# Performance work log

Hardware: AMD Instinct MI355X
Metric: run time of the kernel (lower is better)

Reference implementation:

```python
import jax, jax.numpy as jnp
import numpy as np

B, TX, TY = 32, 64, 64
E = H = 1024
VEN = VCN = 32000


def _lstm_scan(x_gates, Whh, bhh, h0, c0):
    # x_gates: [T, B, 4H] precomputed input contribution (x @ Wih.T + bih)
    def step(carry, xg_t):
        h, c = carry
        gates = xg_t + h @ Whh.T + bhh  # [B, 4H]
        i, f, g, o = jnp.split(gates, 4, axis=-1)  # torch gate order i,f,g,o
        c = jax.nn.sigmoid(f) * c + jax.nn.sigmoid(i) * jnp.tanh(g)
        h = jax.nn.sigmoid(o) * jnp.tanh(c)
        return (h, c), (h, c)
    (hT, cT), (hs, cs) = jax.lax.scan(step, (h0, c0), x_gates)
    return hs, cs, hT, cT  # hs/cs: [T, B, H]


def setup_inputs() -> dict:
    key = jax.random.key(0)
    ks = jax.random.split(key, 12)
    u = lambda k, shp, s: jax.random.uniform(k, shp, jnp.float32, -s, s)
    s = 1.0 / np.sqrt(H)
    return {
        "x": jax.random.randint(ks[0], (B, TX), 0, VEN, dtype=jnp.int32),
        "x_mask": jnp.ones((B, TX), dtype=jnp.int32),
        "y": jax.random.randint(ks[1], (B, TY), 0, VCN, dtype=jnp.int32),
        "h0": jnp.zeros((B, H), jnp.float32),
        "c0": jnp.zeros((B, H), jnp.float32),
        "emb_en": u(ks[2], (VEN, E), 0.1),
        "emb_cn": u(ks[3], (VCN, E), 0.1),
        "Wih_e": u(ks[4], (4 * H, E), s),
        "Whh_e": u(ks[5], (4 * H, H), s),
        "bih_e": jnp.zeros((4 * H,), jnp.float32),
        "bhh_e": jnp.zeros((4 * H,), jnp.float32),
        "Wih_d": u(ks[6], (4 * H, E), s),
        "Whh_d": u(ks[7], (4 * H, H), s),
        "bih_d": jnp.zeros((4 * H,), jnp.float32),
        "bhh_d": jnp.zeros((4 * H,), jnp.float32),
        "Wout": u(ks[8], (VCN, H), 0.1),
        "bout": jnp.zeros((VCN,), jnp.float32),
    }


def reference(x, x_mask, y, h0, c0, emb_en, emb_cn,
              Wih_e, Whh_e, bih_e, bhh_e,
              Wih_d, Whh_d, bih_d, bhh_d, Wout, bout):
    # --- encoder: per-timestep LSTMCell unrolled via lax.scan ---
    xe = emb_en[x]  # [B, Tx, E]
    xg = jnp.einsum('bte,ge->tbg', xe, Wih_e) + bih_e  # [Tx, B, 4H]
    hs, cs, _, _ = _lstm_scan(xg, Whh_e, bhh_e, h0, c0)  # [Tx, B, H]
    # pick hidden/cell at last valid timestep (mask.sum - 1)
    lengths = jnp.sum(x_mask, axis=1) - 1  # [B]
    bidx = jnp.arange(x.shape[0])
    h = hs[lengths, bidx]  # [B, H]
    c = cs[lengths, bidx]
    # --- decoder: single-layer LSTM ---
    ye = emb_cn[y]  # [B, Ty, E]
    yg = jnp.einsum('bte,ge->tbg', ye, Wih_d) + bih_d  # [Ty, B, 4H]
    dh, _, _, _ = _lstm_scan(yg, Whh_d, bhh_d, h, c)  # [Ty, B, H]
    hiddens = jnp.transpose(dh, (1, 0, 2))  # [B, Ty, H]
    logits = jnp.einsum('bth,vh->btv', hiddens, Wout) + bout  # [B, Ty, V]
    decoded = jax.nn.log_softmax(logits, axis=-1)
    return decoded, hiddens
```

## Files before the change

### kernel.cpp

```cpp
#include <hip/hip_runtime.h>

typedef __attribute__((ext_vector_type(8))) short bf16x8;
typedef __attribute__((ext_vector_type(4))) float fx4;
typedef __attribute__((ext_vector_type(4))) unsigned short u16x4;
typedef __attribute__((ext_vector_type(8))) unsigned short u16x8;
typedef __attribute__((ext_vector_type(4))) unsigned int u32x4;

#define DEV static __device__ __forceinline__

DEV unsigned short f2bf(float f) {
  union { float f; unsigned u; } v; v.f = f;
  unsigned u = v.u;
  u += 0x7fffu + ((u >> 16) & 1u);
  return (unsigned short)(u >> 16);
}
DEV unsigned pk(float a, float b) { return (unsigned)f2bf(a) | ((unsigned)f2bf(b) << 16); }
DEV float sigm(float x) { return 1.f / (1.f + __expf(-x)); }

DEV u32x4 load_coh16(const void* p) {
  u32x4 r;
  asm volatile("global_load_dwordx4 %0, %1, off sc0 sc1" : "=v"(r) : "v"(p));
  return r;
}

typedef __attribute__((address_space(1))) const unsigned int guint;
typedef __attribute__((address_space(3))) unsigned int luint;
DEV void gload_lds16(const void* g, void* l) {
  __builtin_amdgcn_global_load_lds((guint*)g, (luint*)l, 16, 0, 0);
}

__global__ void k_gather2(const float* __restrict__ embE, const int* __restrict__ tokE,
                          unsigned short* __restrict__ dstE,
                          const float* __restrict__ embC, const int* __restrict__ tokC,
                          unsigned short* __restrict__ dstC) {
  int bid = blockIdx.x;
  int r = bid & 2047;
  const float* emb = bid < 2048 ? embE : embC;
  const int* tok = bid < 2048 ? tokE : tokC;
  unsigned short* dst = bid < 2048 ? dstE : dstC;
  int t = r >> 5, b = r & 31;
  int token = tok[b * 64 + t];
  const fx4* srow = (const fx4*)(emb + (long)token * 1024);
  u16x4* drow = (u16x4*)(dst + (long)r * 1024);
  fx4 v = srow[threadIdx.x];
  u16x4 o = { f2bf(v[0]), f2bf(v[1]), f2bf(v[2]), f2bf(v[3]) };
  drow[threadIdx.x] = o;
}

__global__ void k_lengths(const int* __restrict__ mask, int* __restrict__ sel,
                          int* __restrict__ bar) {
  int t = threadIdx.x;
  for (int i = t; i < 4096; i += 256) bar[i] = 0;
  if (t < 32) {
    int s = 0;
    for (int k = 0; k < 64; ++k) s += mask[t * 64 + k];
    sel[t] = (s + 63) & 63;
  }
}

__global__ void k_f2bf_dual(const float* __restrict__ s0, unsigned short* __restrict__ d0,
                            const float* __restrict__ s1, unsigned short* __restrict__ d1,
                            long n4) {
  const float* s = blockIdx.x < 1024 ? s0 : s1;
  unsigned short* d = blockIdx.x < 1024 ? d0 : d1;
  long base = (long)(blockIdx.x & 1023) * 256 + threadIdx.x;
  for (long i = base; i < n4; i += 1024 * 256) {
    fx4 v = ((const fx4*)s)[i];
    u16x4 o = { f2bf(v[0]), f2bf(v[1]), f2bf(v[2]), f2bf(v[3]) };
    ((u16x4*)d)[i] = o;
  }
}

#define SCAN_NBLK 64

__global__ __launch_bounds__(512) void k_scan_all(
    const float* __restrict__ WhhE, const float* __restrict__ bhhE,
    const float* __restrict__ xg_e,
    const float* __restrict__ WhhD, const float* __restrict__ bhhD,
    const float* __restrict__ xg_d,
    const float* __restrict__ h0, const float* __restrict__ c0,
    unsigned short* __restrict__ hbuf,
    const int* __restrict__ sel,
    float* __restrict__ hid_out,
    unsigned short* __restrict__ hid_bf,
    int* __restrict__ bar,
    const float* __restrict__ wsrc,
    unsigned short* __restrict__ wdst,
    long wn4) {
  int tid = threadIdx.x;
  int bid = blockIdx.x;
  if (bid >= SCAN_NBLK) {
    long i = (long)(bid - SCAN_NBLK) * 512 + tid;
    long st = (long)(gridDim.x - SCAN_NBLK) * 512;
    for (; i < wn4; i += st) {
      fx4 v = ((const fx4*)wsrc)[i];
      u16x4 o = { f2bf(v[0]), f2bf(v[1]), f2bf(v[2]), f2bf(v[3]) };
      ((u16x4*)wdst)[i] = o;
    }
    return;
  }
  __shared__ __align__(16) unsigned short hlds[49152];
  __shared__ float gbuf[4][32][16];
  int j0 = ((bid & 7) * 8 + (bid >> 3)) * 16;
  int w = tid >> 6, lane = tid & 63;
  int mt = w & 1, nt = w >> 1;
  int fr = lane & 15, fg = lane >> 4;
  unsigned* hbU = (unsigned*)hbuf;

  auto gridbar = [&](int gen) {
    __syncthreads();
    if (w == 0) {
      if (lane == 0)
        __hip_atomic_store(&bar[bid * 32], gen, __ATOMIC_RELAXED, __HIP_MEMORY_SCOPE_AGENT);
      for (;;) {
        int v0 = __hip_atomic_load(&bar[lane * 32], __ATOMIC_RELAXED, __HIP_MEMORY_SCOPE_AGENT);
        if (__ballot(v0 >= gen) == 0xFFFFFFFFFFFFFFFFULL) break;
        __builtin_amdgcn_s_sleep(1);
      }
    }
    __syncthreads();
  };

  auto loadBreg = [&](const float* Whh, bf16x8* breg) {
    const float* wrow = Whh + ((long)(nt * 1024 + j0 + fr) << 10);
#pragma unroll
    for (int i = 0; i < 32; ++i) {
      int kc = i * 4 + fg;
      fx4 lo = *(const fx4*)(wrow + kc * 8);
      fx4 hi = *(const fx4*)(wrow + kc * 8 + 4);
      bf16x8 o = { (short)f2bf(lo[0]), (short)f2bf(lo[1]), (short)f2bf(lo[2]), (short)f2bf(lo[3]),
                   (short)f2bf(hi[0]), (short)f2bf(hi[1]), (short)f2bf(hi[2]), (short)f2bf(hi[3]) };
      breg[i] = o;
    }
  };

  bf16x8 breg[32];
  loadBreg(WhhE, breg);

  int b = tid >> 4, jj = tid & 15, j = j0 + jj;
  float bh0 = bhhE[j], bh1 = bhhE[1024 + j], bh2 = bhhE[2048 + j], bh3 = bhhE[3072 + j];
  float c_reg = c0[b * 1024 + j];
  int sel_b = sel[b];
  float hsel_reg = 0.f, csel_reg = 0.f;
  const float* xp0 = xg_e + (long)b * 4096 + j;
  float x0 = xp0[0], x1 = xp0[1024], x2 = xp0[2048], x3 = xp0[3072];

  for (int t = 0; t < 64; ++t) {
    if (t == 0) {
#pragma unroll
      for (int it = 0; it < 8; ++it) {
        int c = it * 512 + tid;
        const float* src = h0 + (long)c * 8;
        fx4 lo = *(const fx4*)src;
        fx4 hi = *(const fx4*)(src + 4);
        int row = c >> 7, kc = c & 127;
        u16x8 o = { f2bf(lo[0]), f2bf(lo[1]), f2bf(lo[2]), f2bf(lo[3]),
                    f2bf(hi[0]), f2bf(hi[1]), f2bf(hi[2]), f2bf(hi[3]) };
        *(u16x8*)&hlds[(row * 128 + (kc ^ (row & 31))) * 8] = o;
      }
    } else {
      const char* hsrc = (const char*)hbuf + (t & 1) * 65536;
      u32x4 hv[8];
#pragma unroll
      for (int it = 0; it < 8; ++it) {
        int c = it * 512 + tid;
        hv[it] = load_coh16(hsrc + (long)c * 16);
      }
      asm volatile("s_waitcnt vmcnt(0)" ::: "memory");
      __builtin_amdgcn_sched_barrier(0);
#pragma unroll
      for (int it = 0; it < 8; ++it) {
        int c = it * 512 + tid;
        int row = c >> 7, kc = c & 127;
        *(u16x8*)&hlds[(row * 128 + (kc ^ (row & 31))) * 8] = *(u16x8*)&hv[it];
      }
    }
    __syncthreads();

    int arow = mt * 16 + fr;
    fx4 acca = {0.f, 0.f, 0.f, 0.f}, accb = {0.f, 0.f, 0.f, 0.f};
#pragma unroll
    for (int i = 0; i < 32; i += 2) {
      int kcA = i * 4 + fg, kcB = (i + 1) * 4 + fg;
      bf16x8 a0 = *(const bf16x8*)&hlds[(arow * 128 + (kcA ^ (arow & 31))) * 8];
      bf16x8 a1 = *(const bf16x8*)&hlds[(arow * 128 + (kcB ^ (arow & 31))) * 8];
      acca = __builtin_amdgcn_mfma_f32_16x16x32_bf16(a0, breg[i], acca, 0, 0, 0);
      accb = __builtin_amdgcn_mfma_f32_16x16x32_bf16(a1, breg[i + 1], accb, 0, 0, 0);
    }
#pragma unroll
    for (int q = 0; q < 4; ++q)
      gbuf[nt][mt * 16 + fg * 4 + q][fr] = acca[q] + accb[q];
    __syncthreads();

    {
      float gi = gbuf[0][b][jj] + bh0 + x0;
      float gf = gbuf[1][b][jj] + bh1 + x1;
      float gg = gbuf[2][b][jj] + bh2 + x2;
      float go = gbuf[3][b][jj] + bh3 + x3;
      float c_new = sigm(gf) * c_reg + sigm(gi) * tanhf(gg);
      float h = sigm(go) * tanhf(c_new);
      c_reg = c_new;
      float hp = __shfl_xor(h, 1);
      if ((jj & 1) == 0) {
        __hip_atomic_store(&hbU[((t & 1) ^ 1) * 16384 + b * 512 + ((j0 + jj) >> 1)],
                           pk(h, hp), __ATOMIC_RELAXED, __HIP_MEMORY_SCOPE_AGENT);
      }
      if (t == sel_b) { hsel_reg = h; csel_reg = c_new; }
    }

    if (t < 63) {
      const float* xp = xg_e + (long)(t + 1) * 131072 + (long)b * 4096 + j;
      float nx0 = xp[0], nx1 = xp[1024], nx2 = xp[2048], nx3 = xp[3072];
      gridbar(t + 1);
      x0 = nx0; x1 = nx1; x2 = nx2; x3 = nx3;
    }
  }

  loadBreg(WhhD, breg);
  bh0 = bhhD[j]; bh1 = bhhD[1024 + j]; bh2 = bhhD[2048 + j]; bh3 = bhhD[3072 + j];
  c_reg = csel_reg;
  {
    float hp = __shfl_xor(hsel_reg, 1);
    if ((jj & 1) == 0)
      __hip_atomic_store(&hbU[b * 512 + ((j0 + jj) >> 1)],
                         pk(hsel_reg, hp), __ATOMIC_RELAXED, __HIP_MEMORY_SCOPE_AGENT);
  }
  {
    const float* xp = xg_d + (long)b * 4096 + j;
    x0 = xp[0]; x1 = xp[1024]; x2 = xp[2048]; x3 = xp[3072];
  }
  gridbar(64);

  for (int t2 = 0; t2 < 64; ++t2) {
    const char* hsrc = (const char*)hbuf + (t2 & 1) * 65536;
    u32x4 hv[8];
#pragma unroll
    for (int it = 0; it < 8; ++it) {
      int c = it * 512 + tid;
      hv[it] = load_coh16(hsrc + (long)c * 16);
    }
    asm volatile("s_waitcnt vmcnt(0)" ::: "memory");
    __builtin_amdgcn_sched_barrier(0);
#pragma unroll
    for (int it = 0; it < 8; ++it) {
      int c = it * 512 + tid;
      int row = c >> 7, kc = c & 127;
      *(u16x8*)&hlds[(row * 128 + (kc ^ (row & 31))) * 8] = *(u16x8*)&hv[it];
    }
    __syncthreads();

    int arow = mt * 16 + fr;
    fx4 acca = {0.f, 0.f, 0.f, 0.f}, accb = {0.f, 0.f, 0.f, 0.f};
#pragma unroll
    for (int i = 0; i < 32; i += 2) {
      int kcA = i * 4 + fg, kcB = (i + 1) * 4 + fg;
      bf16x8 a0 = *(const bf16x8*)&hlds[(arow * 128 + (kcA ^ (arow & 31))) * 8];
      bf16x8 a1 = *(const bf16x8*)&hlds[(arow * 128 + (kcB ^ (arow & 31))) * 8];
      acca = __builtin_amdgcn_mfma_f32_16x16x32_bf16(a0, breg[i], acca, 0, 0, 0);
      accb = __builtin_amdgcn_mfma_f32_16x16x32_bf16(a1, breg[i + 1], accb, 0, 0, 0);
    }
#pragma unroll
    for (int q = 0; q < 4; ++q)
      gbuf[nt][mt * 16 + fg * 4 + q][fr] = acca[q] + accb[q];
    __syncthreads();

    {
      float gi = gbuf[0][b][jj] + bh0 + x0;
      float gf = gbuf[1][b][jj] + bh1 + x1;
      float gg = gbuf[2][b][jj] + bh2 + x2;
      float go = gbuf[3][b][jj] + bh3 + x3;
      float c_new = sigm(gf) * c_reg + sigm(gi) * tanhf(gg);
      float h = sigm(go) * tanhf(c_new);
      c_reg = c_new;
      float hp = __shfl_xor(h, 1);
      if ((jj & 1) == 0) {
        __hip_atomic_store(&hbU[((t2 & 1) ^ 1) * 16384 + b * 512 + ((j0 + jj) >> 1)],
                           pk(h, hp), __ATOMIC_RELAXED, __HIP_MEMORY_SCOPE_AGENT);
      }
      long o = ((long)b * 64 + t2) * 1024 + j;
      hid_out[o] = h;
      if (hid_bf) hid_bf[o] = f2bf(h);
    }

    if (t2 < 63) {
      const float* xp = xg_d + (long)(t2 + 1) * 131072 + (long)b * 4096 + j;
      float nx0 = xp[0], nx1 = xp[1024], nx2 = xp[2048], nx3 = xp[3072];
      gridbar(65 + t2);
      x0 = nx0; x1 = nx1; x2 = nx2; x3 = nx3;
    }
  }
}

__global__ __launch_bounds__(256) void k_gemm_dual(
    const unsigned short* __restrict__ A0, const unsigned short* __restrict__ B0,
    const float* __restrict__ bias0, float* __restrict__ C0,
    const unsigned short* __restrict__ A1, const unsigned short* __restrict__ B1,
    const float* __restrict__ bias1, float* __restrict__ C1) {
  __shared__ __align__(16) unsigned short As[2][4096];
  __shared__ __align__(16) unsigned short Bs[2][4096];
  int lid = blockIdx.x;
  int half = lid >> 9, l = lid & 511;
  const unsigned short* A = half ? A1 : A0;
  const unsigned short* Bw = half ? B1 : B0;
  const float* bias = half ? bias1 : bias0;
  float* C = half ? C1 : C0;
  int swz = (l & 7) * 64 + (l >> 3);
  long m0 = (long)(swz & 15) * 128;
  long n0 = (long)(swz >> 4) * 128;
  int tid = threadIdx.x, lane = tid & 63, w = tid >> 6;
  int mw = (w & 1) * 64, nw = (w >> 1) * 64;
  int fr = lane & 15, fg = lane >> 4;
  fx4 acc[4][4] = {};
  int c0 = tid, c1 = tid + 256;
  int r0 = c0 >> 2, k0s = (c0 & 3) ^ ((r0 >> 1) & 3);
  int r1 = c1 >> 2, k1s = (c1 & 3) ^ ((r1 >> 1) & 3);
  const unsigned short* gA0 = A + (m0 + r0) * 1024 + k0s * 8;
  const unsigned short* gA1 = A + (m0 + r1) * 1024 + k1s * 8;
  const unsigned short* gB0 = Bw + (n0 + r0) * 1024 + k0s * 8;
  const unsigned short* gB1 = Bw + (n0 + r1) * 1024 + k1s * 8;
  auto stage = [&](int buf, int kt) {
    int k0 = kt * 32;
    gload_lds16(gA0 + k0, &As[buf][c0 * 8]);
    gload_lds16(gA1 + k0, &As[buf][c1 * 8]);
    gload_lds16(gB0 + k0, &Bs[buf][c0 * 8]);
    gload_lds16(gB1 + k0, &Bs[buf][c1 * 8]);
  };
  stage(0, 0);
  __syncthreads();
  for (int kt = 0; kt < 32; ++kt) {
    int cur = kt & 1;
    if (kt < 31) stage(cur ^ 1, kt + 1);
    bf16x8 af[4], bfr[4];
#pragma unroll
    for (int mi = 0; mi < 4; ++mi) {
      int row = mw + mi * 16 + fr;
      af[mi] = *(const bf16x8*)&As[cur][(row * 4 + (fg ^ ((row >> 1) & 3))) * 8];
    }
#pragma unroll
    for (int ni = 0; ni < 4; ++ni) {
      int row = nw + ni * 16 + fr;
      bfr[ni] = *(const bf16x8*)&Bs[cur][(row * 4 + (fg ^ ((row >> 1) & 3))) * 8];
    }
#pragma unroll
    for (int mi = 0; mi < 4; ++mi)
#pragma unroll
      for (int ni = 0; ni < 4; ++ni)
        acc[mi][ni] = __builtin_amdgcn_mfma_f32_16x16x32_bf16(af[mi], bfr[ni], acc[mi][ni], 0, 0, 0);
    __syncthreads();
  }
#pragma unroll
  for (int ni = 0; ni < 4; ++ni) {
    long n = n0 + nw + ni * 16 + fr;
    float bs = bias[n];
#pragma unroll
    for (int mi = 0; mi < 4; ++mi) {
      long rbase = m0 + mw + mi * 16 + fg * 4;
#pragma unroll
      for (int q = 0; q < 4; ++q)
        C[(rbase + q) * 4096 + n] = acc[mi][ni][q] + bs;
    }
  }
}

__global__ __launch_bounds__(256) void k_gemm_bb(const unsigned short* __restrict__ A,
                                                 const unsigned short* __restrict__ Bw,
                                                 const float* __restrict__ bias,
                                                 float* __restrict__ C) {
  __shared__ __align__(16) unsigned short As[2][4096];
  __shared__ __align__(16) unsigned short Bs[2][4096];
  int lid = blockIdx.x;
  int swz = (lid & 7) * 500 + (lid >> 3);
  long m0 = (long)(swz / 250) * 128;
  long n0 = (long)(swz % 250) * 128;
  int tid = threadIdx.x, lane = tid & 63, w = tid >> 6;
  int mw = (w & 1) * 64, nw = (w >> 1) * 64;
  int fr = lane & 15, fg = lane >> 4;
  fx4 acc[4][4] = {};
  int c0 = tid, c1 = tid + 256;
  int r0 = c0 >> 2, k0s = (c0 & 3) ^ ((r0 >> 1) & 3);
  int r1 = c1 >> 2, k1s = (c1 & 3) ^ ((r1 >> 1) & 3);
  const unsigned short* gA0 = A + (m0 + r0) * 1024 + k0s * 8;
  const unsigned short* gA1 = A + (m0 + r1) * 1024 + k1s * 8;
  const unsigned short* gB0 = Bw + (n0 + r0) * 1024 + k0s * 8;
  const unsigned short* gB1 = Bw + (n0 + r1) * 1024 + k1s * 8;
  auto stage = [&](int buf, int kt) {
    int k0 = kt * 32;
    gload_lds16(gA0 + k0, &As[buf][c0 * 8]);
    gload_lds16(gA1 + k0, &As[buf][c1 * 8]);
    gload_lds16(gB0 + k0, &Bs[buf][c0 * 8]);
    gload_lds16(gB1 + k0, &Bs[buf][c1 * 8]);
  };
  stage(0, 0);
  __syncthreads();
  for (int kt = 0; kt < 32; ++kt) {
    int cur = kt & 1;
    if (kt < 31) stage(cur ^ 1, kt + 1);
    bf16x8 af[4], bfr[4];
#pragma unroll
    for (int mi = 0; mi < 4; ++mi) {
      int row = mw + mi * 16 + fr;
      af[mi] = *(const bf16x8*)&As[cur][(row * 4 + (fg ^ ((row >> 1) & 3))) * 8];
    }
#pragma unroll
    for (int ni = 0; ni < 4; ++ni) {
      int row = nw + ni * 16 + fr;
      bfr[ni] = *(const bf16x8*)&Bs[cur][(row * 4 + (fg ^ ((row >> 1) & 3))) * 8];
    }
#pragma unroll
    for (int mi = 0; mi < 4; ++mi)
#pragma unroll
      for (int ni = 0; ni < 4; ++ni)
        acc[mi][ni] = __builtin_amdgcn_mfma_f32_16x16x32_bf16(bfr[ni], af[mi], acc[mi][ni], 0, 0, 0);
    __syncthreads();
  }
#pragma unroll
  for (int mi = 0; mi < 4; ++mi) {
    long m = m0 + mw + mi * 16 + fr;
#pragma unroll
    for (int ni = 0; ni < 4; ++ni) {
      long nbase = n0 + nw + ni * 16 + fg * 4;
      fx4 bs4 = *(const fx4*)&bias[nbase];
      fx4 o = { acc[mi][ni][0] + bs4[0], acc[mi][ni][1] + bs4[1],
                acc[mi][ni][2] + bs4[2], acc[mi][ni][3] + bs4[3] };
      *(fx4*)&C[m * 32000 + nbase] = o;
    }
  }
}

template<typename TA, typename TB>
__global__ __launch_bounds__(256) void k_gemm(const TA* __restrict__ A,
                                              const TB* __restrict__ Bw,
                                              const float* __restrict__ bias,
                                              float* __restrict__ C,
                                              int ldc, int q8) {
  __shared__ __align__(16) unsigned short As[2][4096];
  __shared__ __align__(16) unsigned short Bs[2][4096];
  int lid = blockIdx.x;
  int swz = (lid & 7) * q8 + (lid >> 3);
  long m0 = (long)(swz & 15) * 128;
  long n0 = (long)(swz >> 4) * 128;
  int tid = threadIdx.x, lane = tid & 63, w = tid >> 6;
  int mw = (w & 1) * 64, nw = (w >> 1) * 64;
  int fr = lane & 15, fg = lane >> 4;
  fx4 acc[4][4] = {};

  int crow[2], kc[2], phys[2];
#pragma unroll
  for (int u = 0; u < 2; ++u) {
    int c = tid + u * 256;
    crow[u] = c >> 2; kc[u] = c & 3;
    phys[u] = crow[u] * 4 + (kc[u] ^ ((crow[u] >> 1) & 3));
  }
  u32x4 ra[2], rb[2];
  auto loadOne = [&](const auto* P, long row, int u) -> u32x4 {
    long off = row * 1024 + kc[u] * 8;
    if constexpr (sizeof(*P) == 2) {
      return *(const u32x4*)(P + off);
    } else {
      fx4 lo = *(const fx4*)(P + off);
      fx4 hi = *(const fx4*)(P + off + 4);
      u32x4 r = { pk(lo[0], lo[1]), pk(lo[2], lo[3]), pk(hi[0], hi[1]), pk(hi[2], hi[3]) };
      return r;
    }
  };
  auto loadRegs = [&](int kt) {
#pragma unroll
    for (int u = 0; u < 2; ++u) {
      ra[u] = loadOne(A + (long)kt * 32, m0 + crow[u], u);
      rb[u] = loadOne(Bw + (long)kt * 32, n0 + crow[u], u);
    }
  };
  auto storeRegs = [&](int buf) {
#pragma unroll
    for (int u = 0; u < 2; ++u) {
      *(u32x4*)&As[buf][phys[u] * 8] = ra[u];
      *(u32x4*)&Bs[buf][phys[u] * 8] = rb[u];
    }
  };
  loadRegs(0);
  storeRegs(0);
  __syncthreads();
  for (int kt = 0; kt < 32; ++kt) {
    int cur = kt & 1;
    if (kt < 31) loadRegs(kt + 1);
    bf16x8 af[4], bf_[4];
#pragma unroll
    for (int mi = 0; mi < 4; ++mi) {
      int row = mw + mi * 16 + fr;
      af[mi] = *(const bf16x8*)&As[cur][(row * 4 + (fg ^ ((row >> 1) & 3))) * 8];
    }
#pragma unroll
    for (int ni = 0; ni < 4; ++ni) {
      int row = nw + ni * 16 + fr;
      bf_[ni] = *(const bf16x8*)&Bs[cur][(row * 4 + (fg ^ ((row >> 1) & 3))) * 8];
    }
#pragma unroll
    for (int mi = 0; mi < 4; ++mi)
#pragma unroll
      for (int ni = 0; ni < 4; ++ni)
        acc[mi][ni] = __builtin_amdgcn_mfma_f32_16x16x32_bf16(af[mi], bf_[ni], acc[mi][ni], 0, 0, 0);
    if (kt < 31) storeRegs((kt + 1) & 1);
    __syncthreads();
  }
#pragma unroll
  for (int ni = 0; ni < 4; ++ni) {
    long n = n0 + nw + ni * 16 + fr;
    float bs = bias[n];
#pragma unroll
    for (int mi = 0; mi < 4; ++mi) {
      long rbase = m0 + mw + mi * 16 + fg * 4;
#pragma unroll
      for (int q = 0; q < 4; ++q)
        C[(rbase + q) * ldc + n] = acc[mi][ni][q] + bs;
    }
  }
}

__global__ __launch_bounds__(256) void k_logsoftmax(float* __restrict__ logits) {
  long base = (long)blockIdx.x * 32000;
  float* row = logits + base;
  int tid = threadIdx.x;
  __shared__ float redm[4], reds[4];
  float m = -3.4e38f, s = 0.f;
  for (int i = tid; i < 8000; i += 256) {
    fx4 v = ((const fx4*)row)[i];
    float cm = fmaxf(fmaxf(v[0], v[1]), fmaxf(v[2], v[3]));
    if (cm > m) { s *= __expf(m - cm); m = cm; }
    s += __expf(v[0] - m) + __expf(v[1] - m) + __expf(v[2] - m) + __expf(v[3] - m);
  }
  for (int o = 32; o; o >>= 1) {
    float m2 = __shfl_xor(m, o), s2 = __shfl_xor(s, o);
    float mn = fmaxf(m, m2);
    s = s * __expf(m - mn) + s2 * __expf(m2 - mn);
    m = mn;
  }
  if ((tid & 63) == 0) { redm[tid >> 6] = m; reds[tid >> 6] = s; }
  __syncthreads();
  float M = fmaxf(fmaxf(redm[0], redm[1]), fmaxf(redm[2], redm[3]));
  float S = reds[0] * __expf(redm[0] - M) + reds[1] * __expf(redm[1] - M) +
            reds[2] * __expf(redm[2] - M) + reds[3] * __expf(redm[3] - M);
  float lse = M + logf(S);
  for (int i = tid; i < 8000; i += 256) {
    fx4 v = ((const fx4*)row)[i];
    fx4 o = { v[0] - lse, v[1] - lse, v[2] - lse, v[3] - lse };
    ((fx4*)row)[i] = o;
  }
}

extern "C" void kernel_launch(void* const* d_in, const int* in_sizes, int n_in,
                              void* d_out, int out_size, void* d_ws, size_t ws_size,
                              hipStream_t stream) {
  const int*   x     = (const int*)d_in[0];
  const int*   xmask = (const int*)d_in[1];
  const int*   y     = (const int*)d_in[2];
  const float* h0    = (const float*)d_in[3];
  const float* c0    = (const float*)d_in[4];
  const float* embE  = (const float*)d_in[5];
  const float* embC  = (const float*)d_in[6];
  const float* WihE  = (const float*)d_in[7];
  const float* WhhE  = (const float*)d_in[8];
  const float* bihE  = (const float*)d_in[9];
  const float* bhhE  = (const float*)d_in[10];
  const float* WihD  = (const float*)d_in[11];
  const float* WhhD  = (const float*)d_in[12];
  const float* bihD  = (const float*)d_in[13];
  const float* bhhD  = (const float*)d_in[14];
  const float* Wout  = (const float*)d_in[15];
  const float* bout  = (const float*)d_in[16];

  float* out = (float*)d_out;
  float* decoded = out;
  float* hiddens = out + 65536000L;

  float* xg_e = decoded;
  float* xg_d = decoded + 8388608L;
  unsigned short* xe_bf   = (unsigned short*)(decoded + 16777216L);
  unsigned short* ye_bf   = xe_bf + 2097152L;
  unsigned short* WihE_bf = ye_bf + 2097152L;
  unsigned short* WihD_bf = WihE_bf + 4194304L;
  char* sp = (char*)(WihD_bf + 4194304L);
  unsigned short* hbuf = (unsigned short*)sp; sp += 2 * 32768 * 2;
  int* sel = (int*)sp; sp += 256;
  int* bar = (int*)sp; sp += 16384;

  unsigned short* hid_bf  = (unsigned short*)d_ws;
  unsigned short* Wout_bf = hid_bf + 2097152L;
  size_t need1 = 2048L * 1024 * 2;
  size_t need2 = need1 + 32000L * 1024 * 2;
  bool fast1 = ws_size >= need1;
  bool fast2 = ws_size >= need2;

  k_lengths<<<1, 256, 0, stream>>>(xmask, sel, bar);
  k_gather2<<<4096, 256, 0, stream>>>(embE, x, xe_bf, embC, y, ye_bf);
  k_f2bf_dual<<<2048, 256, 0, stream>>>(WihE, WihE_bf, WihD, WihD_bf, 1048576L);

  k_gemm_dual<<<1024, 256, 0, stream>>>(xe_bf, WihE_bf, bihE, xg_e,
                                        ye_bf, WihD_bf, bihD, xg_d);

  k_scan_all<<<SCAN_NBLK + (fast2 ? 192 : 0), 512, 0, stream>>>(
      WhhE, bhhE, xg_e, WhhD, bhhD, xg_d, h0, c0, hbuf, sel, hiddens,
      fast1 ? hid_bf : nullptr, bar, Wout, Wout_bf, fast2 ? 8192000L : 0L);

  if (fast2)      k_gemm_bb<<<4000, 256, 0, stream>>>(hid_bf, Wout_bf, bout, decoded);
  else if (fast1) k_gemm<unsigned short, float><<<4000, 256, 0, stream>>>(hid_bf, Wout, bout, decoded, 32000, 500);
  else            k_gemm<float, float><<<4000, 256, 0, stream>>>(hiddens, Wout, bout, decoded, 32000, 500);
  k_logsoftmax<<<2048, 256, 0, stream>>>(decoded);
}
```

Baseline: 922.4 us.

## Replace grid barrier with step-tagged hidden-state flags in persistent LSTM scan

```diff
diff --git a/kernel.cpp b/kernel.cpp
--- a/kernel.cpp
+++ b/kernel.cpp
@@ -47,12 +47,13 @@
   drow[threadIdx.x] = o;
 }
 
-__global__ void k_lengths(const int* __restrict__ mask, int* __restrict__ sel,
-                          int* __restrict__ bar) {
-  int t = threadIdx.x;
-  for (int i = t; i < 4096; i += 256) bar[i] = 0;
-  if (t < 32) {
-    int s = 0;
+__global__ void k_init(const int* __restrict__ mask, int* __restrict__ sel,
+                       unsigned* __restrict__ hbufT) {
+  int i = blockIdx.x * 256 + threadIdx.x;
+  u32x4 z = {0u, 0u, 0u, 0u};
+  ((u32x4*)hbufT)[i] = z;
+  if (blockIdx.x == 0 && threadIdx.x < 32) {
+    int t = threadIdx.x, s = 0;
     for (int k = 0; k < 64; ++k) s += mask[t * 64 + k];
     sel[t] = (s + 63) & 63;
   }
@@ -79,11 +80,10 @@
     const float* __restrict__ WhhD, const float* __restrict__ bhhD,
     const float* __restrict__ xg_d,
     const float* __restrict__ h0, const float* __restrict__ c0,
-    unsigned short* __restrict__ hbuf,
+    unsigned* __restrict__ hbufT,
     const int* __restrict__ sel,
     float* __restrict__ hid_out,
     unsigned short* __restrict__ hid_bf,
-    int* __restrict__ bar,
     const float* __restrict__ wsrc,
     unsigned short* __restrict__ wdst,
     long wn4) {
@@ -105,21 +105,6 @@
   int w = tid >> 6, lane = tid & 63;
   int mt = w & 1, nt = w >> 1;
   int fr = lane & 15, fg = lane >> 4;
-  unsigned* hbU = (unsigned*)hbuf;
-
-  auto gridbar = [&](int gen) {
-    __syncthreads();
-    if (w == 0) {
-      if (lane == 0)
-        __hip_atomic_store(&bar[bid * 32], gen, __ATOMIC_RELAXED, __HIP_MEMORY_SCOPE_AGENT);
-      for (;;) {
-        int v0 = __hip_atomic_load(&bar[lane * 32], __ATOMIC_RELAXED, __HIP_MEMORY_SCOPE_AGENT);
-        if (__ballot(v0 >= gen) == 0xFFFFFFFFFFFFFFFFULL) break;
-        __builtin_amdgcn_s_sleep(1);
-      }
-    }
-    __syncthreads();
-  };
 
   auto loadBreg = [&](const float* Whh, bf16x8* breg) {
     const float* wrow = Whh + ((long)(nt * 1024 + j0 + fr) << 10);
@@ -131,6 +116,49 @@
       bf16x8 o = { (short)f2bf(lo[0]), (short)f2bf(lo[1]), (short)f2bf(lo[2]), (short)f2bf(lo[3]),
                    (short)f2bf(hi[0]), (short)f2bf(hi[1]), (short)f2bf(hi[2]), (short)f2bf(hi[3]) };
       breg[i] = o;
+    }
+  };
+
+  int colb = (tid & 255) * 4;
+  int kcs = colb >> 3, sub = (colb & 7) * 2;
+  auto stage_tagged = [&](int s) {
+    const unsigned* src = hbufT + (s & 1) * 32768;
+    u32x4 hv[16];
+#pragma unroll
+    for (int it = 0; it < 16; ++it)
+      hv[it] = load_coh16(src + it * 2048 + tid * 4);
+    asm volatile("s_waitcnt vmcnt(0)" ::: "memory");
+    unsigned stale = 0;
+#pragma unroll
+    for (int it = 0; it < 16; ++it) {
+      unsigned bad = 0;
+#pragma unroll
+      for (int e = 0; e < 4; ++e) bad |= ((hv[it][e] & 0xffffu) < (unsigned)s) ? 1u : 0u;
+      stale |= bad << it;
+    }
+    while (stale) {
+      __builtin_amdgcn_s_sleep(1);
+      for (int it = 0; it < 16; ++it)
+        if (stale & (1u << it))
+          hv[it] = load_coh16(src + it * 2048 + tid * 4);
+      asm volatile("s_waitcnt vmcnt(0)" ::: "memory");
+      unsigned ns = 0;
+      for (int it = 0; it < 16; ++it) {
+        if (stale & (1u << it)) {
+          unsigned bad = 0;
+          for (int e = 0; e < 4; ++e) bad |= ((hv[it][e] & 0xffffu) < (unsigned)s) ? 1u : 0u;
+          ns |= bad << it;
+        }
+      }
+      stale = ns;
+    }
+    __builtin_amdgcn_sched_barrier(0);
+#pragma unroll
+    for (int it = 0; it < 16; ++it) {
+      int row = it * 2 + (tid >> 8);
+      u16x4 o = { (unsigned short)(hv[it][0] >> 16), (unsigned short)(hv[it][1] >> 16),
+                  (unsigned short)(hv[it][2] >> 16), (unsigned short)(hv[it][3] >> 16) };
+      *(u16x4*)((char*)hlds + (row * 128 + (kcs ^ (row & 31))) * 16 + sub) = o;
     }
   };
 
@@ -159,21 +187,7 @@
         *(u16x8*)&hlds[(row * 128 + (kc ^ (row & 31))) * 8] = o;
       }
     } else {
-      const char* hsrc = (const char*)hbuf + (t & 1) * 65536;
-      u32x4 hv[8];
-#pragma unroll
-      for (int it = 0; it < 8; ++it) {
-        int c = it * 512 + tid;
-        hv[it] = load_coh16(hsrc + (long)c * 16);
-      }
-      asm volatile("s_waitcnt vmcnt(0)" ::: "memory");
-      __builtin_amdgcn_sched_barrier(0);
-#pragma unroll
-      for (int it = 0; it < 8; ++it) {
-        int c = it * 512 + tid;
-        int row = c >> 7, kc = c & 127;
-        *(u16x8*)&hlds[(row * 128 + (kc ^ (row & 31))) * 8] = *(u16x8*)&hv[it];
-      }
+      stage_tagged(t);
     }
     __syncthreads();
 
@@ -200,53 +214,24 @@
       float c_new = sigm(gf) * c_reg + sigm(gi) * tanhf(gg);
       float h = sigm(go) * tanhf(c_new);
       c_reg = c_new;
-      float hp = __shfl_xor(h, 1);
-      if ((jj & 1) == 0) {
-        __hip_atomic_store(&hbU[((t & 1) ^ 1) * 16384 + b * 512 + ((j0 + jj) >> 1)],
-                           pk(h, hp), __ATOMIC_RELAXED, __HIP_MEMORY_SCOPE_AGENT);
-      }
       if (t == sel_b) { hsel_reg = h; csel_reg = c_new; }
-    }
-
-    if (t < 63) {
-      const float* xp = xg_e + (long)(t + 1) * 131072 + (long)b * 4096 + j;
-      float nx0 = xp[0], nx1 = xp[1024], nx2 = xp[2048], nx3 = xp[3072];
-      gridbar(t + 1);
-      x0 = nx0; x1 = nx1; x2 = nx2; x3 = nx3;
-    }
+      float hw = (t == 63) ? hsel_reg : h;
+      unsigned val = ((unsigned)f2bf(hw) << 16) | (unsigned)(t + 1);
+      __hip_atomic_store(&hbufT[((t + 1) & 1) * 32768 + b * 1024 + j], val,
+                         __ATOMIC_RELAXED, __HIP_MEMORY_SCOPE_AGENT);
+    }
+
+    const float* xp = (t < 63) ? (xg_e + (long)(t + 1) * 131072 + (long)b * 4096 + j)
+                               : (xg_d + (long)b * 4096 + j);
+    x0 = xp[0]; x1 = xp[1024]; x2 = xp[2048]; x3 = xp[3072];
   }
 
   loadBreg(WhhD, breg);
   bh0 = bhhD[j]; bh1 = bhhD[1024 + j]; bh2 = bhhD[2048 + j]; bh3 = bhhD[3072 + j];
   c_reg = csel_reg;
-  {
-    float hp = __shfl_xor(hsel_reg, 1);
-    if ((jj & 1) == 0)
-      __hip_atomic_store(&hbU[b * 512 + ((j0 + jj) >> 1)],
-                         pk(hsel_reg, hp), __ATOMIC_RELAXED, __HIP_MEMORY_SCOPE_AGENT);
-  }
-  {
-    const float* xp = xg_d + (long)b * 4096 + j;
-    x0 = xp[0]; x1 = xp[1024]; x2 = xp[2048]; x3 = xp[3072];
-  }
-  gridbar(64);
 
   for (int t2 = 0; t2 < 64; ++t2) {
-    const char* hsrc = (const char*)hbuf + (t2 & 1) * 65536;
-    u32x4 hv[8];
-#pragma unroll
-    for (int it = 0; it < 8; ++it) {
-      int c = it * 512 + tid;
-      hv[it] = load_coh16(hsrc + (long)c * 16);
-    }
-    asm volatile("s_waitcnt vmcnt(0)" ::: "memory");
-    __builtin_amdgcn_sched_barrier(0);
-#pragma unroll
-    for (int it = 0; it < 8; ++it) {
-      int c = it * 512 + tid;
-      int row = c >> 7, kc = c & 127;
-      *(u16x8*)&hlds[(row * 128 + (kc ^ (row & 31))) * 8] = *(u16x8*)&hv[it];
-    }
+    stage_tagged(64 + t2);
     __syncthreads();
 
     int arow = mt * 16 + fr;
@@ -272,10 +257,11 @@
       float c_new = sigm(gf) * c_reg + sigm(gi) * tanhf(gg);
       float h = sigm(go) * tanhf(c_new);
       c_reg = c_new;
-      float hp = __shfl_xor(h, 1);
-      if ((jj & 1) == 0) {
-        __hip_atomic_store(&hbU[((t2 & 1) ^ 1) * 16384 + b * 512 + ((j0 + jj) >> 1)],
-                           pk(h, hp), __ATOMIC_RELAXED, __HIP_MEMORY_SCOPE_AGENT);
+      int s = 64 + t2;
+      if (t2 < 63) {
+        unsigned val = ((unsigned)f2bf(h) << 16) | (unsigned)(s + 1);
+        __hip_atomic_store(&hbufT[((s + 1) & 1) * 32768 + b * 1024 + j], val,
+                           __ATOMIC_RELAXED, __HIP_MEMORY_SCOPE_AGENT);
       }
       long o = ((long)b * 64 + t2) * 1024 + j;
       hid_out[o] = h;
@@ -284,9 +270,7 @@
 
     if (t2 < 63) {
       const float* xp = xg_d + (long)(t2 + 1) * 131072 + (long)b * 4096 + j;
-      float nx0 = xp[0], nx1 = xp[1024], nx2 = xp[2048], nx3 = xp[3072];
-      gridbar(65 + t2);
-      x0 = nx0; x1 = nx1; x2 = nx2; x3 = nx3;
+      x0 = xp[0]; x1 = xp[1024]; x2 = xp[2048]; x3 = xp[3072];
     }
   }
 }
@@ -579,9 +563,8 @@
   unsigned short* WihE_bf = ye_bf + 2097152L;
   unsigned short* WihD_bf = WihE_bf + 4194304L;
   char* sp = (char*)(WihD_bf + 4194304L);
-  unsigned short* hbuf = (unsigned short*)sp; sp += 2 * 32768 * 2;
+  unsigned* hbufT = (unsigned*)sp; sp += 65536 * 4;
   int* sel = (int*)sp; sp += 256;
-  int* bar = (int*)sp; sp += 16384;
 
   unsigned short* hid_bf  = (unsigned short*)d_ws;
   unsigned short* Wout_bf = hid_bf + 2097152L;
@@ -590,7 +573,7 @@
   bool fast1 = ws_size >= need1;
   bool fast2 = ws_size >= need2;
 
-  k_lengths<<<1, 256, 0, stream>>>(xmask, sel, bar);
+  k_init<<<64, 256, 0, stream>>>(xmask, sel, hbufT);
   k_gather2<<<4096, 256, 0, stream>>>(embE, x, xe_bf, embC, y, ye_bf);
   k_f2bf_dual<<<2048, 256, 0, stream>>>(WihE, WihE_bf, WihD, WihD_bf, 1048576L);
 
@@ -598,8 +581,8 @@
                                         ye_bf, WihD_bf, bihD, xg_d);
 
   k_scan_all<<<SCAN_NBLK + (fast2 ? 192 : 0), 512, 0, stream>>>(
-      WhhE, bhhE, xg_e, WhhD, bhhD, xg_d, h0, c0, hbuf, sel, hiddens,
-      fast1 ? hid_bf : nullptr, bar, Wout, Wout_bf, fast2 ? 8192000L : 0L);
+      WhhE, bhhE, xg_e, WhhD, bhhD, xg_d, h0, c0, hbufT, sel, hiddens,
+      fast1 ? hid_bf : nullptr, Wout, Wout_bf, fast2 ? 8192000L : 0L);
 
   if (fast2)      k_gemm_bb<<<4000, 256, 0, stream>>>(hid_bf, Wout_bf, bout, decoded);
   else if (fast1) k_gemm<unsigned short, float><<<4000, 256, 0, stream>>>(hid_bf, Wout, bout, decoded, 32000, 500);
```

Result: slower. 1.398 ms (+51.6%).
